# Performance work log

Measured on AMD Instinct MI355X. Metric: run time of the kernel, lower is better.

## Reference

```python
import jax, jax.numpy as jnp
import numpy as np

NUM_GRAPHS = 128


def _gcn_layer(x, W, b, src, dst, out_norm, in_norm, n_nodes):
    # DGL GraphConv, norm='both': x * outdeg^{-1/2}, sum-aggregate src->dst, * indeg^{-1/2}, then @W + b
    x = x * out_norm[:, None]
    agg = jax.ops.segment_sum(x[src], dst, num_segments=n_nodes)  # [N, d]
    agg = agg * in_norm[:, None]
    return agg @ W + b


def setup_inputs() -> dict:
    key = jax.random.key(0)
    ks = jax.random.split(key, 10)
    N, E, D, H, P, C = 100000, 1600000, 128, 128, 64, 10
    h = jax.random.normal(ks[0], (N, D), dtype=jnp.float32)
    perm_features = jax.random.normal(ks[1], (NUM_GRAPHS, P), dtype=jnp.float32)
    W1 = jax.random.normal(ks[2], (D, H), dtype=jnp.float32) * (1.0 / np.sqrt(D))
    b1 = jnp.zeros((H,), dtype=jnp.float32)
    W2 = jax.random.normal(ks[3], (H, H), dtype=jnp.float32) * (1.0 / np.sqrt(H))
    b2 = jnp.zeros((H,), dtype=jnp.float32)
    Wc = jax.random.normal(ks[4], (H + P, C), dtype=jnp.float32) * (1.0 / np.sqrt(H + P))
    bc = jnp.zeros((C,), dtype=jnp.float32)
    src = jax.random.randint(ks[5], (E,), 0, N, dtype=jnp.int64)
    dst = jax.random.randint(ks[6], (E,), 0, N, dtype=jnp.int64)
    graph_ids = jnp.sort(jax.random.randint(ks[7], (N,), 0, NUM_GRAPHS, dtype=jnp.int64))
    return {"h": h, "perm_features": perm_features, "W1": W1, "b1": b1,
            "W2": W2, "b2": b2, "Wc": Wc, "bc": bc,
            "src": src, "dst": dst, "graph_ids": graph_ids}


def reference(h, perm_features, W1, b1, W2, b2, Wc, bc, src, dst, graph_ids):
    N = h.shape[0]
    ones_e = jnp.ones(src.shape[0], dtype=h.dtype)
    out_deg = jnp.maximum(jax.ops.segment_sum(ones_e, src, num_segments=N), 1.0)
    in_deg = jnp.maximum(jax.ops.segment_sum(ones_e, dst, num_segments=N), 1.0)
    out_norm = jax.lax.rsqrt(out_deg)
    in_norm = jax.lax.rsqrt(in_deg)

    x = _gcn_layer(h, W1, b1, src, dst, out_norm, in_norm, N)
    x = jax.nn.relu(x)
    x = _gcn_layer(x, W2, b2, src, dst, out_norm, in_norm, N)

    # dgl.mean_nodes: per-graph mean of node features
    sums = jax.ops.segment_sum(x, graph_ids, num_segments=NUM_GRAPHS)  # [G, H]
    counts = jnp.maximum(
        jax.ops.segment_sum(jnp.ones(N, dtype=x.dtype), graph_ids, num_segments=NUM_GRAPHS), 1.0)
    hg = sums / counts[:, None]

    combined = jnp.concatenate([hg, perm_features], axis=1)  # [G, H+P]
    return combined @ Wc + bc
```

## Files before the change

### kernel.cpp

```cpp
#include <hip/hip_runtime.h>


#define NUM_G 128
#define PB_EDGES 4096
#define W_BIN 128

typedef unsigned int uint32;
typedef short bf16x8 __attribute__((ext_vector_type(8)));
typedef float f32x4 __attribute__((ext_vector_type(4)));

__device__ __forceinline__ float bflo(uint32 u) { return __uint_as_float(u << 16); }
__device__ __forceinline__ float bfhi(uint32 u) { return __uint_as_float(u & 0xffff0000u); }
__device__ __forceinline__ uint32 f2bf_bits(float f) {
    uint32 b = __float_as_uint(f);
    return (b + 0x7fffu + ((b >> 16) & 1u)) >> 16;
}
__device__ __forceinline__ uint32 pack2(float a, float b) {
    return f2bf_bits(a) | (f2bf_bits(b) << 16);
}

__global__ __launch_bounds__(256) void p1_hist(const int* __restrict__ src,
                                               const int* __restrict__ dst, int E,
                                               int NBIN, int B, int* __restrict__ bh) {
    __shared__ int hist[1024];
    int b = blockIdx.x;
    int pipe = (b >= B) ? 1 : 0;
    int bb = pipe ? b - B : b;
    const int* key = pipe ? src : dst;
    for (int i = threadIdx.x; i < NBIN; i += 256) hist[i] = 0;
    __syncthreads();
    int base = bb * PB_EDGES;
    for (int c = threadIdx.x; c < PB_EDGES / 4; c += 256) {
        int e = base + c * 4;
        if (e + 3 < E) {
            int4 k4 = *(const int4*)(key + e);
            atomicAdd(&hist[k4.x >> 7], 1);
            atomicAdd(&hist[k4.y >> 7], 1);
            atomicAdd(&hist[k4.z >> 7], 1);
            atomicAdd(&hist[k4.w >> 7], 1);
        } else {
            for (int i = e; i < E && i < e + 4; i++) atomicAdd(&hist[key[i] >> 7], 1);
        }
    }
    __syncthreads();
    int* outp = bh + (size_t)pipe * NBIN * B;
    for (int k = threadIdx.x; k < NBIN; k += 256)
        outp[(size_t)k * B + bb] = hist[k];
}

__global__ __launch_bounds__(256) void p2a_tot(const int* __restrict__ bh, int NBIN, int B,
                                               int* __restrict__ tot) {
    __shared__ int sc[256];
    int k = blockIdx.x % NBIN, pipe = blockIdx.x / NBIN;
    const int* row = bh + (size_t)pipe * NBIN * B + (size_t)k * B;
    int acc = 0;
    for (int b = threadIdx.x; b < B; b += 256) acc += row[b];
    sc[threadIdx.x] = acc;
    __syncthreads();
    for (int o = 128; o > 0; o >>= 1) {
        if (threadIdx.x < o) sc[threadIdx.x] += sc[threadIdx.x + o];
        __syncthreads();
    }
    if (threadIdx.x == 0) tot[pipe * NBIN + k] = sc[0];
}

__global__ __launch_bounds__(512) void p2c_cursor(const int* __restrict__ bh,
                                                  const int* __restrict__ tot,
                                                  int NBIN, int B, int E,
                                                  int* __restrict__ bstart,
                                                  int* __restrict__ curs) {
    __shared__ int sc[512];
    int k = blockIdx.x % NBIN, pipe = blockIdx.x / NBIN;
    int i = threadIdx.x;
    int pacc = 0;
    for (int kk = i; kk < k; kk += 512) pacc += tot[pipe * NBIN + kk];
    sc[i] = pacc;
    __syncthreads();
    for (int o = 256; o > 0; o >>= 1) {
        if (i < o) sc[i] += sc[i + o];
        __syncthreads();
    }
    int base = sc[0];
    __syncthreads();
    if (i == 0) {
        bstart[pipe * (NBIN + 1) + k] = base;
        if (k == 0) bstart[pipe * (NBIN + 1) + NBIN] = E;
    }
    const int* row = bh + (size_t)pipe * NBIN * B + (size_t)k * B;
    int v = (i < B) ? row[i] : 0;
    sc[i] = v;
    __syncthreads();
    for (int o = 1; o < 512; o <<= 1) {
        int t = (i >= o) ? sc[i - o] : 0;
        __syncthreads();
        sc[i] += t;
        __syncthreads();
    }
    if (i < B)
        curs[(size_t)pipe * B * NBIN + (size_t)i * NBIN + k] = base + sc[i] - v;
}

__global__ __launch_bounds__(256) void p3_scatter(const int* __restrict__ src,
                                                  const int* __restrict__ dst, int E,
                                                  int NBIN, int B, const int* __restrict__ curs,
                                                  int2* __restrict__ ebuf, int* __restrict__ sbuf) {
    __shared__ int cur[1024];
    int b = blockIdx.x;
    int pipe = (b >= B) ? 1 : 0;
    int bb = pipe ? b - B : b;
    const int* crow = curs + (size_t)pipe * B * NBIN + (size_t)bb * NBIN;
    for (int i = threadIdx.x; i < NBIN; i += 256) cur[i] = crow[i];
    __syncthreads();
    int base = bb * PB_EDGES;
    if (!pipe) {
        for (int c = threadIdx.x; c < PB_EDGES / 4; c += 256) {
            int e = base + c * 4;
            if (e + 3 < E) {
                int4 s4 = *(const int4*)(src + e);
                int4 d4 = *(const int4*)(dst + e);
                int p;
                p = atomicAdd(&cur[d4.x >> 7], 1); ebuf[p] = make_int2(s4.x, d4.x);
                p = atomicAdd(&cur[d4.y >> 7], 1); ebuf[p] = make_int2(s4.y, d4.y);
                p = atomicAdd(&cur[d4.z >> 7], 1); ebuf[p] = make_int2(s4.z, d4.z);
                p = atomicAdd(&cur[d4.w >> 7], 1); ebuf[p] = make_int2(s4.w, d4.w);
            } else {
                for (int i = e; i < E && i < e + 4; i++) {
                    int s = src[i], d = dst[i];
                    int p = atomicAdd(&cur[d >> 7], 1);
                    ebuf[p] = make_int2(s, d);
                }
            }
        }
    } else {
        for (int c = threadIdx.x; c < PB_EDGES / 4; c += 256) {
            int e = base + c * 4;
            if (e + 3 < E) {
                int4 s4 = *(const int4*)(src + e);
                int p;
                p = atomicAdd(&cur[s4.x >> 7], 1); sbuf[p] = s4.x;
                p = atomicAdd(&cur[s4.y >> 7], 1); sbuf[p] = s4.y;
                p = atomicAdd(&cur[s4.z >> 7], 1); sbuf[p] = s4.z;
                p = atomicAdd(&cur[s4.w >> 7], 1); sbuf[p] = s4.w;
            } else {
                for (int i = e; i < E && i < e + 4; i++) {
                    int s = src[i];
                    int p = atomicAdd(&cur[s >> 7], 1);
                    sbuf[p] = s;
                }
            }
        }
    }
}

__global__ __launch_bounds__(256) void p4_comb(const int2* __restrict__ ebuf,
                                               const int* __restrict__ sbuf,
                                               const int* __restrict__ bstart,
                                               int NBIN, int N, int E,
                                               int* __restrict__ indeg, int* __restrict__ coff,
                                               int* __restrict__ adj, int* __restrict__ outdeg) {
    __shared__ int hist[128];
    __shared__ int sc[128];
    __shared__ int cur[128];
    __shared__ int lsrc[4096];
    int kb = blockIdx.x;
    int tid = threadIdx.x;
    if (kb >= NBIN) {
        int k = kb - NBIN;
        const int* bstartS = bstart + (NBIN + 1);
        int s0 = bstartS[k], s1 = bstartS[k + 1];
        if (tid < 128) hist[tid] = 0;
        __syncthreads();
        for (int i = s0 + tid; i < s1; i += 256) atomicAdd(&hist[sbuf[i] & 127], 1);
        __syncthreads();
        if (tid < 128) {
            int node = k * W_BIN + tid;
            if (node < N) outdeg[node] = hist[tid];
        }
        return;
    }
    int k = kb;
    int s0 = bstart[k], s1 = bstart[k + 1];
    int M = s1 - s0;
    if (tid < 128) hist[tid] = 0;
    __syncthreads();
    for (int i = tid; i < M; i += 256) {
        int2 e = ebuf[s0 + i];
        atomicAdd(&hist[e.y & 127], 1);
    }
    __syncthreads();
    if (tid < 128) sc[tid] = hist[tid];
    __syncthreads();
    for (int o = 1; o < 128; o <<= 1) {
        int v = 0;
        if (tid < 128 && tid >= o) v = sc[tid - o];
        __syncthreads();
        if (tid < 128) sc[tid] += v;
        __syncthreads();
    }
    if (tid < 128) {
        int node = k * W_BIN + tid;
        if (node < N) {
            indeg[node] = hist[tid];
            coff[node] = s0 + sc[tid] - hist[tid];
        }
        cur[tid] = sc[tid] - hist[tid];
    }
    if (k == NBIN - 1 && tid == 0) coff[N] = E;
    __syncthreads();
    if (M <= 4096) {
        for (int i = tid; i < M; i += 256) {
            int2 e = ebuf[s0 + i];
            int p = atomicAdd(&cur[e.y & 127], 1);
            lsrc[p] = e.x;
        }
        __syncthreads();
        for (int i = tid; i < M; i += 256) adj[s0 + i] = lsrc[i];
    } else {
        for (int i = tid; i < M; i += 256) {
            int2 e = ebuf[s0 + i];
            int p = atomicAdd(&cur[e.y & 127], 1);
            adj[s0 + p] = e.x;
        }
    }
}

__global__ void misc_kernel(const int* __restrict__ gids,
                            const int* __restrict__ outdeg, const int* __restrict__ indeg,
                            const float* __restrict__ W1, const float* __restrict__ W2,
                            int N, int* __restrict__ goffs,
                            float* __restrict__ nrm_out, float* __restrict__ nrm_in,
                            unsigned short* __restrict__ Wt1, unsigned short* __restrict__ Wt2) {
    int i = blockIdx.x * blockDim.x + threadIdx.x;
    if (i <= N) {
        int prev = (i == 0) ? -1 : gids[i - 1];
        int cur = (i == N) ? NUM_G : gids[i];
        for (int g = prev + 1; g <= cur && g <= NUM_G; g++) goffs[g] = i;
    }
    if (i < N) {
        nrm_out[i] = rsqrtf(fmaxf((float)outdeg[i], 1.0f));
        nrm_in[i]  = rsqrtf(fmaxf((float)indeg[i], 1.0f));
    }
    if (i < 32768) {
        int sel = i >> 14;
        int idx = i & 16383;
        int k = idx >> 7, n = idx & 127;
        float v = (sel ? W2 : W1)[idx];
        (sel ? Wt2 : Wt1)[n * 128 + k] = (unsigned short)f2bf_bits(v);
    }
}

__global__ void scale_kernel(const float* __restrict__ h, const float* __restrict__ nrm_out,
                             uint32* __restrict__ xsb, int N) {
    int t = blockIdx.x * blockDim.x + threadIdx.x;
    int node = t >> 4, q = t & 15;
    if (node >= N) return;
    float ns = nrm_out[node];
    const float4* hv = (const float4*)(h + (size_t)node * 128 + q * 8);
    float4 a = hv[0], b = hv[1];
    a.x *= ns; a.y *= ns; a.z *= ns; a.w *= ns;
    b.x *= ns; b.y *= ns; b.z *= ns; b.w *= ns;
    uint4 o;
    o.x = pack2(a.x, a.y); o.y = pack2(a.z, a.w);
    o.z = pack2(b.x, b.y); o.w = pack2(b.z, b.w);
    ((uint4*)xsb)[(size_t)node * 16 + q] = o;
}

__global__ void agg_kernel(const uint32* __restrict__ xsb, const int* __restrict__ adj,
                           const int* __restrict__ coff, uint32* __restrict__ aggb, int N) {
    int t = blockIdx.x * blockDim.x + threadIdx.x;
    int node = t >> 4;
    int q = t & 15;
    if (node >= N) return;
    int jb = coff[node], je = coff[node + 1];
    float acc[8];
#pragma unroll
    for (int i = 0; i < 8; i++) acc[i] = 0.f;
    const uint4* rows = (const uint4*)xsb;
    int j = jb;
    for (; j + 3 < je; j += 4) {
        int s0 = adj[j], s1 = adj[j + 1], s2 = adj[j + 2], s3 = adj[j + 3];
        uint4 u0 = rows[(size_t)s0 * 16 + q];
        uint4 u1 = rows[(size_t)s1 * 16 + q];
        uint4 u2 = rows[(size_t)s2 * 16 + q];
        uint4 u3 = rows[(size_t)s3 * 16 + q];
        acc[0] += bflo(u0.x); acc[1] += bfhi(u0.x); acc[2] += bflo(u0.y); acc[3] += bfhi(u0.y);
        acc[4] += bflo(u0.z); acc[5] += bfhi(u0.z); acc[6] += bflo(u0.w); acc[7] += bfhi(u0.w);
        acc[0] += bflo(u1.x); acc[1] += bfhi(u1.x); acc[2] += bflo(u1.y); acc[3] += bfhi(u1.y);
        acc[4] += bflo(u1.z); acc[5] += bfhi(u1.z); acc[6] += bflo(u1.w); acc[7] += bfhi(u1.w);
        acc[0] += bflo(u2.x); acc[1] += bfhi(u2.x); acc[2] += bflo(u2.y); acc[3] += bfhi(u2.y);
        acc[4] += bflo(u2.z); acc[5] += bfhi(u2.z); acc[6] += bflo(u2.w); acc[7] += bfhi(u2.w);
        acc[0] += bflo(u3.x); acc[1] += bfhi(u3.x); acc[2] += bflo(u3.y); acc[3] += bfhi(u3.y);
        acc[4] += bflo(u3.z); acc[5] += bfhi(u3.z); acc[6] += bflo(u3.w); acc[7] += bfhi(u3.w);
    }
    for (; j < je; j++) {
        int s = adj[j];
        uint4 u = rows[(size_t)s * 16 + q];
        acc[0] += bflo(u.x); acc[1] += bfhi(u.x); acc[2] += bflo(u.y); acc[3] += bfhi(u.y);
        acc[4] += bflo(u.z); acc[5] += bfhi(u.z); acc[6] += bflo(u.w); acc[7] += bfhi(u.w);
    }
    uint4 o;
    o.x = pack2(acc[0], acc[1]); o.y = pack2(acc[2], acc[3]);
    o.z = pack2(acc[4], acc[5]); o.w = pack2(acc[6], acc[7]);
    ((uint4*)aggb)[(size_t)node * 16 + q] = o;
}

__global__ __launch_bounds__(256) void gemm_mfma(const unsigned short* __restrict__ A,
                                                 const unsigned short* __restrict__ Wtg,
                                                 const float* __restrict__ bias,
                                                 const float* __restrict__ rowscale,
                                                 const float* __restrict__ postscale,
                                                 unsigned short* __restrict__ out,
                                                 int N, int do_relu) {
    __shared__ unsigned short Wl[128 * 136];
    for (int i = threadIdx.x; i < 2048; i += 256) {
        uint4 v = ((const uint4*)Wtg)[i];
        *(uint4*)&Wl[(i >> 4) * 136 + (i & 15) * 8] = v;
    }
    __syncthreads();

    int lane = threadIdx.x & 63;
    int wv = threadIdx.x >> 6;
    int col_l = lane & 15;
    int quad = lane >> 4;
    int r0w = blockIdx.x * 128 + wv * 32;
    if (r0w >= N) return;

    int arow0 = r0w + col_l;        if (arow0 >= N) arow0 = N - 1;
    int arow1 = r0w + 16 + col_l;   if (arow1 >= N) arow1 = N - 1;
    const unsigned short* Ar0 = A + (size_t)arow0 * 128;
    const unsigned short* Ar1 = A + (size_t)arow1 * 128;

    f32x4 acc[2][8];
#pragma unroll
    for (int rt = 0; rt < 2; rt++)
#pragma unroll
        for (int t = 0; t < 8; t++) {
            acc[rt][t][0] = 0.f; acc[rt][t][1] = 0.f;
            acc[rt][t][2] = 0.f; acc[rt][t][3] = 0.f;
        }

#pragma unroll
    for (int kk = 0; kk < 4; kk++) {
        bf16x8 a0 = *(const bf16x8*)(Ar0 + kk * 32 + quad * 8);
        bf16x8 a1 = *(const bf16x8*)(Ar1 + kk * 32 + quad * 8);
        const unsigned short* wb = &Wl[(size_t)col_l * 136 + kk * 32 + quad * 8];
#pragma unroll
        for (int t = 0; t < 8; t++) {
            bf16x8 b = *(const bf16x8*)(wb + (size_t)t * 16 * 136);
            acc[0][t] = __builtin_amdgcn_mfma_f32_16x16x32_bf16(a0, b, acc[0][t], 0, 0, 0);
            acc[1][t] = __builtin_amdgcn_mfma_f32_16x16x32_bf16(a1, b, acc[1][t], 0, 0, 0);
        }
    }

#pragma unroll
    for (int rt = 0; rt < 2; rt++) {
        int rbase = r0w + rt * 16;
        float s[4], p[4];
#pragma unroll
        for (int j = 0; j < 4; j++) {
            int rw = rbase + quad * 4 + j;
            bool ok = rw < N;
            s[j] = ok ? rowscale[ok ? rw : 0] : 0.f;
            p[j] = (postscale != nullptr && ok) ? postscale[rw] : 1.f;
        }
#pragma unroll
        for (int t = 0; t < 8; t++) {
            int c = t * 16 + col_l;
            float bia = bias[c];
#pragma unroll
            for (int j = 0; j < 4; j++) {
                int rw = rbase + quad * 4 + j;
                if (rw >= N) continue;
                float v = fmaf(s[j], acc[rt][t][j], bia);
                if (do_relu) v = fmaxf(v, 0.f);
                v *= p[j];
                out[(size_t)rw * 128 + c] = (unsigned short)f2bf_bits(v);
            }
        }
    }
}

__global__ __launch_bounds__(1024) void mean_final(const uint32* __restrict__ x2b,
                                                   const int* __restrict__ goffs,
                                                   const float* __restrict__ perm,
                                                   const float* __restrict__ Wc,
                                                   const float* __restrict__ bc,
                                                   float* __restrict__ out) {
    __shared__ float red[16][128];
    __shared__ float hrow[128];
    int g = blockIdx.x;
    int cp = threadIdx.x & 63;
    int j = threadIdx.x >> 6;
    int s = goffs[g], e = goffs[g + 1];
    float a0 = 0.f, a1 = 0.f;
    for (int r = s + j; r < e; r += 16) {
        uint32 u = x2b[(size_t)r * 64 + cp];
        a0 += bflo(u); a1 += bfhi(u);
    }
    red[j][cp * 2] = a0;
    red[j][cp * 2 + 1] = a1;
    __syncthreads();
    if (j == 0) {
        float t0 = 0.f, t1 = 0.f;
#pragma unroll
        for (int jj = 0; jj < 16; jj++) { t0 += red[jj][cp * 2]; t1 += red[jj][cp * 2 + 1]; }
        float cnt = fmaxf((float)(e - s), 1.0f);
        hrow[cp * 2] = t0 / cnt;
        hrow[cp * 2 + 1] = t1 / cnt;
    }
    __syncthreads();
    if (threadIdx.x < 10) {
        int c = threadIdx.x;
        float acc = bc[c];
#pragma unroll 8
        for (int k = 0; k < 128; k++) acc = fmaf(hrow[k], Wc[k * 10 + c], acc);
        const float* prow = perm + g * 64;
#pragma unroll 8
        for (int p = 0; p < 64; p++) acc = fmaf(prow[p], Wc[(128 + p) * 10 + c], acc);
        out[g * 10 + c] = acc;
    }
}

extern "C" void kernel_launch(void* const* d_in, const int* in_sizes, int n_in,
                              void* d_out, int out_size, void* d_ws, size_t ws_size,
                              hipStream_t stream) {
    const float* h    = (const float*)d_in[0];
    const float* perm = (const float*)d_in[1];
    const float* W1   = (const float*)d_in[2];
    const float* b1   = (const float*)d_in[3];
    const float* W2   = (const float*)d_in[4];
    const float* b2   = (const float*)d_in[5];
    const float* Wc   = (const float*)d_in[6];
    const float* bc   = (const float*)d_in[7];
    const int* src    = (const int*)d_in[8];
    const int* dst    = (const int*)d_in[9];
    const int* gids   = (const int*)d_in[10];
    float* out = (float*)d_out;

    const int N = in_sizes[0] / 128;
    const int E = in_sizes[8];
    const int G = NUM_G, H = 128;
    const int B = (E + PB_EDGES - 1) / PB_EDGES;
    const int NBIN = (N + W_BIN - 1) / W_BIN;

    char* w = (char*)d_ws;
    size_t off = 0;
    auto alloc = [&](size_t bytes) -> void* {
        void* p = w + off;
        off = (off + bytes + 255) & ~(size_t)255;
        return p;
    };
    uint32* xsb   = (uint32*)alloc((size_t)N * H * 2);
    uint32* aggb  = (uint32*)alloc((size_t)N * H * 2);
    uint32* x1b   = (uint32*)alloc((size_t)N * H * 2);
    unsigned short* Wt1 = (unsigned short*)alloc(16384 * 2);
    unsigned short* Wt2 = (unsigned short*)alloc(16384 * 2);
    int*    adj     = (int*)alloc((size_t)E * 4);
    int*    coff    = (int*)alloc((size_t)(N + 1) * 4);
    int*    indeg   = (int*)alloc((size_t)N * 4);
    int*    outdeg  = (int*)alloc((size_t)N * 4);
    float*  nrm_out = (float*)alloc((size_t)N * 4);
    float*  nrm_in  = (float*)alloc((size_t)N * 4);
    int*    goffs   = (int*)alloc((size_t)(G + 1) * 4);

    char* tmp = (char*)aggb;
    size_t toff = 0;
    auto talloc = [&](size_t bytes) -> void* {
        void* p = tmp + toff;
        toff = (toff + bytes + 255) & ~(size_t)255;
        return p;
    };
    int2* ebuf   = (int2*)talloc((size_t)E * 8);
    int*  sbuf   = (int*)talloc((size_t)E * 4);
    int*  bh     = (int*)talloc((size_t)2 * B * NBIN * 4);
    int*  curs   = (int*)talloc((size_t)2 * B * NBIN * 4);
    int*  tot    = (int*)talloc((size_t)2 * NBIN * 4);
    int*  bstart = (int*)talloc((size_t)2 * (NBIN + 1) * 4);

    p1_hist<<<2 * B, 256, 0, stream>>>(src, dst, E, NBIN, B, bh);
    p2a_tot<<<2 * NBIN, 256, 0, stream>>>(bh, NBIN, B, tot);
    p2c_cursor<<<2 * NBIN, 512, 0, stream>>>(bh, tot, NBIN, B, E, bstart, curs);
    p3_scatter<<<2 * B, 256, 0, stream>>>(src, dst, E, NBIN, B, curs, ebuf, sbuf);
    p4_comb<<<2 * NBIN, 256, 0, stream>>>(ebuf, sbuf, bstart, NBIN, N, E,
                                          indeg, coff, adj, outdeg);

    misc_kernel<<<(N + 1 + 255) / 256, 256, 0, stream>>>(gids, outdeg, indeg, W1, W2, N,
                                                         goffs, nrm_out, nrm_in, Wt1, Wt2);

    scale_kernel<<<(N * 16 + 255) / 256, 256, 0, stream>>>(h, nrm_out, xsb, N);
    agg_kernel<<<(N * 16 + 255) / 256, 256, 0, stream>>>(xsb, adj, coff, aggb, N);
    gemm_mfma<<<(N + 127) / 128, 256, 0, stream>>>((const unsigned short*)aggb, Wt1, b1,
                                                   nrm_in, nrm_out,
                                                   (unsigned short*)x1b, N, 1);

    agg_kernel<<<(N * 16 + 255) / 256, 256, 0, stream>>>(x1b, adj, coff, aggb, N);
    gemm_mfma<<<(N + 127) / 128, 256, 0, stream>>>((const unsigned short*)aggb, Wt2, b2,
                                                   nrm_in, nullptr,
                                                   (unsigned short*)xsb, N, 0);

    mean_final<<<G, 1024, 0, stream>>>(xsb, goffs, perm, Wc, bc, out);
}
```

Before: 354.4 us.

## Store node features in column-chunked layout to localize gather working set

Node feature buffers are re-laid out into 8 column chunks of 16 bf16 each (chunk-major), and the aggregation kernel assigns each block to a single chunk, so concurrently running blocks gather from a 3.2MB slice instead of the full row array. The scale, aggregation and first GEMM kernels are adapted to read and write this chunked layout, while the second GEMM still writes row-major for the mean kernel. The aim is better L2/cache hit rates on the random neighbor gathers. In exchange, each gather now fetches only 32 bytes per node per thread pair and the adjacency list is re-read once per chunk.

Result: slower. 442.1 us (+24.8%).

```diff
diff --git a/kernel.cpp b/kernel.cpp
--- a/kernel.cpp
+++ b/kernel.cpp
@@ -249,40 +249,44 @@
     }
 }
 
-__global__ void scale_kernel(const float* __restrict__ h, const float* __restrict__ nrm_out,
-                             uint32* __restrict__ xsb, int N) {
-    int t = blockIdx.x * blockDim.x + threadIdx.x;
-    int node = t >> 4, q = t & 15;
+__global__ __launch_bounds__(256) void scale_kernel(const float* __restrict__ h,
+                                                    const float* __restrict__ nrm_out,
+                                                    uint32* __restrict__ xsb, int N) {
+    int c = blockIdx.x & 7;
+    int node = (blockIdx.x >> 3) * 128 + (threadIdx.x >> 1);
+    int half = threadIdx.x & 1;
     if (node >= N) return;
     float ns = nrm_out[node];
-    const float4* hv = (const float4*)(h + (size_t)node * 128 + q * 8);
+    const float4* hv = (const float4*)(h + (size_t)node * 128 + c * 16 + half * 8);
     float4 a = hv[0], b = hv[1];
     a.x *= ns; a.y *= ns; a.z *= ns; a.w *= ns;
     b.x *= ns; b.y *= ns; b.z *= ns; b.w *= ns;
     uint4 o;
     o.x = pack2(a.x, a.y); o.y = pack2(a.z, a.w);
     o.z = pack2(b.x, b.y); o.w = pack2(b.z, b.w);
-    ((uint4*)xsb)[(size_t)node * 16 + q] = o;
-}
-
-__global__ void agg_kernel(const uint32* __restrict__ xsb, const int* __restrict__ adj,
-                           const int* __restrict__ coff, uint32* __restrict__ aggb, int N) {
-    int t = blockIdx.x * blockDim.x + threadIdx.x;
-    int node = t >> 4;
-    int q = t & 15;
+    ((uint4*)xsb)[(size_t)c * N * 2 + (size_t)node * 2 + half] = o;
+}
+
+__global__ __launch_bounds__(256) void agg_kernel(const uint32* __restrict__ xsb,
+                                                  const int* __restrict__ adj,
+                                                  const int* __restrict__ coff,
+                                                  uint32* __restrict__ aggb, int N) {
+    int c = blockIdx.x & 7;
+    int node = (blockIdx.x >> 3) * 128 + (threadIdx.x >> 1);
+    int half = threadIdx.x & 1;
     if (node >= N) return;
     int jb = coff[node], je = coff[node + 1];
+    const uint4* rows = (const uint4*)xsb + (size_t)c * N * 2 + half;
     float acc[8];
 #pragma unroll
     for (int i = 0; i < 8; i++) acc[i] = 0.f;
-    const uint4* rows = (const uint4*)xsb;
     int j = jb;
     for (; j + 3 < je; j += 4) {
         int s0 = adj[j], s1 = adj[j + 1], s2 = adj[j + 2], s3 = adj[j + 3];
-        uint4 u0 = rows[(size_t)s0 * 16 + q];
-        uint4 u1 = rows[(size_t)s1 * 16 + q];
-        uint4 u2 = rows[(size_t)s2 * 16 + q];
-        uint4 u3 = rows[(size_t)s3 * 16 + q];
+        uint4 u0 = rows[(size_t)s0 * 2];
+        uint4 u1 = rows[(size_t)s1 * 2];
+        uint4 u2 = rows[(size_t)s2 * 2];
+        uint4 u3 = rows[(size_t)s3 * 2];
         acc[0] += bflo(u0.x); acc[1] += bfhi(u0.x); acc[2] += bflo(u0.y); acc[3] += bfhi(u0.y);
         acc[4] += bflo(u0.z); acc[5] += bfhi(u0.z); acc[6] += bflo(u0.w); acc[7] += bfhi(u0.w);
         acc[0] += bflo(u1.x); acc[1] += bfhi(u1.x); acc[2] += bflo(u1.y); acc[3] += bfhi(u1.y);
@@ -294,16 +298,17 @@
     }
     for (; j < je; j++) {
         int s = adj[j];
-        uint4 u = rows[(size_t)s * 16 + q];
+        uint4 u = rows[(size_t)s * 2];
         acc[0] += bflo(u.x); acc[1] += bfhi(u.x); acc[2] += bflo(u.y); acc[3] += bfhi(u.y);
         acc[4] += bflo(u.z); acc[5] += bfhi(u.z); acc[6] += bflo(u.w); acc[7] += bfhi(u.w);
     }
     uint4 o;
     o.x = pack2(acc[0], acc[1]); o.y = pack2(acc[2], acc[3]);
     o.z = pack2(acc[4], acc[5]); o.w = pack2(acc[6], acc[7]);
-    ((uint4*)aggb)[(size_t)node * 16 + q] = o;
-}
-
+    ((uint4*)aggb)[(size_t)c * N * 2 + (size_t)node * 2 + half] = o;
+}
+
+template <bool OUT_CHUNKED>
 __global__ __launch_bounds__(256) void gemm_mfma(const unsigned short* __restrict__ A,
                                                  const unsigned short* __restrict__ Wtg,
                                                  const float* __restrict__ bias,
@@ -318,6 +323,7 @@
     }
     __syncthreads();
 
+    const size_t CS = (size_t)N * 16;
     int lane = threadIdx.x & 63;
     int wv = threadIdx.x >> 6;
     int col_l = lane & 15;
@@ -327,8 +333,9 @@
 
     int arow0 = r0w + col_l;        if (arow0 >= N) arow0 = N - 1;
     int arow1 = r0w + 16 + col_l;   if (arow1 >= N) arow1 = N - 1;
-    const unsigned short* Ar0 = A + (size_t)arow0 * 128;
-    const unsigned short* Ar1 = A + (size_t)arow1 * 128;
+    size_t lchunk = (size_t)(quad >> 1) * CS + (quad & 1) * 8;
+    const unsigned short* Ar0 = A + lchunk + (size_t)arow0 * 16;
+    const unsigned short* Ar1 = A + lchunk + (size_t)arow1 * 16;
 
     f32x4 acc[2][8];
 #pragma unroll
@@ -341,8 +348,8 @@
 
 #pragma unroll
     for (int kk = 0; kk < 4; kk++) {
-        bf16x8 a0 = *(const bf16x8*)(Ar0 + kk * 32 + quad * 8);
-        bf16x8 a1 = *(const bf16x8*)(Ar1 + kk * 32 + quad * 8);
+        bf16x8 a0 = *(const bf16x8*)(Ar0 + (size_t)kk * 2 * CS);
+        bf16x8 a1 = *(const bf16x8*)(Ar1 + (size_t)kk * 2 * CS);
         const unsigned short* wb = &Wl[(size_t)col_l * 136 + kk * 32 + quad * 8];
 #pragma unroll
         for (int t = 0; t < 8; t++) {
@@ -374,7 +381,10 @@
                 float v = fmaf(s[j], acc[rt][t][j], bia);
                 if (do_relu) v = fmaxf(v, 0.f);
                 v *= p[j];
-                out[(size_t)rw * 128 + c] = (unsigned short)f2bf_bits(v);
+                if (OUT_CHUNKED)
+                    out[(size_t)t * CS + (size_t)rw * 16 + col_l] = (unsigned short)f2bf_bits(v);
+                else
+                    out[(size_t)rw * 128 + c] = (unsigned short)f2bf_bits(v);
             }
         }
     }
@@ -487,16 +497,18 @@
     misc_kernel<<<(N + 1 + 255) / 256, 256, 0, stream>>>(gids, outdeg, indeg, W1, W2, N,
                                                          goffs, nrm_out, nrm_in, Wt1, Wt2);
 
-    scale_kernel<<<(N * 16 + 255) / 256, 256, 0, stream>>>(h, nrm_out, xsb, N);
-    agg_kernel<<<(N * 16 + 255) / 256, 256, 0, stream>>>(xsb, adj, coff, aggb, N);
-    gemm_mfma<<<(N + 127) / 128, 256, 0, stream>>>((const unsigned short*)aggb, Wt1, b1,
-                                                   nrm_in, nrm_out,
-                                                   (unsigned short*)x1b, N, 1);
-
-    agg_kernel<<<(N * 16 + 255) / 256, 256, 0, stream>>>(x1b, adj, coff, aggb, N);
-    gemm_mfma<<<(N + 127) / 128, 256, 0, stream>>>((const unsigned short*)aggb, Wt2, b2,
-                                                   nrm_in, nullptr,
-                                                   (unsigned short*)xsb, N, 0);
+    const int NG8 = 8 * ((N + 127) / 128);
+
+    scale_kernel<<<NG8, 256, 0, stream>>>(h, nrm_out, xsb, N);
+    agg_kernel<<<NG8, 256, 0, stream>>>(xsb, adj, coff, aggb, N);
+    gemm_mfma<true><<<(N + 127) / 128, 256, 0, stream>>>((const unsigned short*)aggb, Wt1, b1,
+                                                         nrm_in, nrm_out,
+                                                         (unsigned short*)x1b, N, 1);
+
+    agg_kernel<<<NG8, 256, 0, stream>>>(x1b, adj, coff, aggb, N);
+    gemm_mfma<false><<<(N + 127) / 128, 256, 0, stream>>>((const unsigned short*)aggb, Wt2, b2,
+                                                          nrm_in, nullptr,
+                                                          (unsigned short*)xsb, N, 0);
 
     mean_final<<<G, 1024, 0, stream>>>(xsb, goffs, perm, Wc, bc, out);
 }
```
